# Performance work log

Hardware: AMD Instinct MI355X
Metric: run time of the kernel (lower is better)

## Reference

```python
import jax, jax.numpy as jnp
import numpy as np

DIM, NH, T_MAX = 1024, 16, 2048
HD = DIM // NH
EPS = 1e-6


def _rope_tables(T, hd, dtype=jnp.float32):
    inv_freq = 1.0 / (10000.0 ** (jnp.arange(0, hd, 2, dtype=jnp.float32) / hd))
    t = jnp.arange(T, dtype=jnp.float32)
    freqs = jnp.outer(t, inv_freq)                 # [T, hd/2]
    emb = jnp.concatenate([freqs, freqs], axis=-1)  # [T, hd]
    return jnp.cos(emb).astype(dtype), jnp.sin(emb).astype(dtype)


def _rotate_half(x):
    x1, x2 = jnp.split(x, 2, axis=-1)
    return jnp.concatenate([-x2, x1], axis=-1)


def _rmsnorm(x, g):
    rms = jnp.sqrt(jnp.mean(x * x, axis=-1, keepdims=True) + EPS)
    return x / rms * g


def setup_inputs() -> dict:
    key = jax.random.key(0)
    ks = jax.random.split(key, 10)
    B, T, C = 4, 2048, DIM
    s = 1.0 / np.sqrt(C)
    x = jax.random.normal(ks[0], (B, T, C), dtype=jnp.float32)
    mask = jnp.tril(jnp.ones((T, T), dtype=jnp.int32))[None, None, :, :]
    wq = jax.random.normal(ks[1], (C, C), jnp.float32) * s
    wk = jax.random.normal(ks[2], (C, C), jnp.float32) * s
    wv = jax.random.normal(ks[3], (C, C), jnp.float32) * s
    wo = jax.random.normal(ks[4], (C, C), jnp.float32) * s
    w1 = jax.random.normal(ks[5], (C, 4 * C), jnp.float32) * s
    w2 = jax.random.normal(ks[6], (4 * C, C), jnp.float32) * (1.0 / np.sqrt(4 * C))
    w3 = jax.random.normal(ks[7], (C, 4 * C), jnp.float32) * s
    g1 = jnp.ones((C,), jnp.float32)
    g2 = jnp.ones((C,), jnp.float32)
    return {"x": x, "mask": mask, "g1": g1, "wq": wq, "wk": wk, "wv": wv,
            "wo": wo, "g2": g2, "w1": w1, "w2": w2, "w3": w3}


def reference(x, mask, g1, wq, wk, wv, wo, g2, w1, w2, w3):
    B, T, C = x.shape
    scale = HD ** -0.5
    # --- attention sublayer ---
    h = _rmsnorm(x, g1)
    q = (h @ wq).reshape(B, T, NH, HD)
    k = (h @ wk).reshape(B, T, NH, HD)
    v = (h @ wv).reshape(B, T, NH, HD)
    cos, sin = _rope_tables(T, HD, x.dtype)
    cos = cos[None, :, None, :]
    sin = sin[None, :, None, :]
    q = q * cos + _rotate_half(q) * sin
    k = k * cos + _rotate_half(k) * sin
    attn = jnp.einsum("bthd,bshd->bhts", q, k) * scale  # [B,H,T,T]
    attn = jnp.where(mask == 0, -jnp.inf, attn)
    attn = jax.nn.softmax(attn, axis=-1)
    o = jnp.einsum("bhts,bshd->bthd", attn, v).reshape(B, T, C)
    x = x + o @ wo
    # --- SwiGLU FFN sublayer ---
    h = _rmsnorm(x, g2)
    x = x + (jax.nn.silu(h @ w1) * (h @ w3)) @ w2
    return x
```

## Files before the change

### kernel.cpp

```cpp
#include <hip/hip_runtime.h>
#include <cstdint>

typedef unsigned short u16;
typedef __attribute__((ext_vector_type(8))) short bf16x8;
typedef __attribute__((ext_vector_type(4))) float f32x4;

__device__ __forceinline__ u16 f2b(float f) {
  union { float f; unsigned u; } c; c.f = f;
  unsigned u = c.u;
  return (u16)((u + 0x7FFFu + ((u >> 16) & 1u)) >> 16);
}
__device__ __forceinline__ float b2f(u16 b) {
  union { unsigned u; float f; } c; c.u = ((unsigned)b) << 16;
  return c.f;
}

typedef __attribute__((address_space(1))) void gv_t;
typedef __attribute__((address_space(3))) void lv_t;
__device__ __forceinline__ void gload_lds16(const void* g, void* l) {
  __builtin_amdgcn_global_load_lds((gv_t*)g, (lv_t*)l, 16, 0, 0);
}

__global__ void transpose_f2b(const float* __restrict__ in, u16* __restrict__ out,
                              int R, int C) {
  __shared__ float t[32][33];
  const int c0 = blockIdx.x * 32, r0 = blockIdx.y * 32;
  const int tx = threadIdx.x, ty = threadIdx.y;
#pragma unroll
  for (int i = 0; i < 4; ++i)
    t[ty + 8 * i][tx] = in[(size_t)(r0 + ty + 8 * i) * C + c0 + tx];
  __syncthreads();
#pragma unroll
  for (int i = 0; i < 4; ++i)
    out[(size_t)(c0 + ty + 8 * i) * R + r0 + tx] = f2b(t[tx][ty + 8 * i]);
}

__global__ __launch_bounds__(256) void rmsnorm_k(const float* __restrict__ x,
                                                 const float* __restrict__ g,
                                                 u16* __restrict__ out) {
  const int row = blockIdx.x, tid = threadIdx.x;
  const float4 v = ((const float4*)x)[(size_t)row * 256 + tid];
  float ss = v.x * v.x + v.y * v.y + v.z * v.z + v.w * v.w;
#pragma unroll
  for (int off = 1; off < 64; off <<= 1) ss += __shfl_xor(ss, off, 64);
  __shared__ float red[4];
  if ((tid & 63) == 0) red[tid >> 6] = ss;
  __syncthreads();
  const float mean = (red[0] + red[1] + red[2] + red[3]) * (1.0f / 1024.0f);
  const float rinv = 1.0f / sqrtf(mean + 1e-6f);
  const float4 gv = ((const float4*)g)[tid];
  u16* o = out + (size_t)row * 1024 + tid * 4;
  o[0] = f2b(v.x * rinv * gv.x);
  o[1] = f2b(v.y * rinv * gv.y);
  o[2] = f2b(v.z * rinv * gv.z);
  o[3] = f2b(v.w * rinv * gv.w);
}

__global__ __launch_bounds__(256) void rope_k(u16* __restrict__ qkv) {
  const int i = blockIdx.x * 256 + threadIdx.x;
  const int d = i & 31;
  const int h = (i >> 5) & 15;
  const int bt = i >> 9;
  const int t = bt & 2047;
  const float inv = exp2f((float)d * -0.4152410118609203f);
  const float th = (float)t * inv;
  float s, c;
  sincosf(th, &s, &c);
  size_t base = (size_t)bt * 3072 + h * 64 + d;
#pragma unroll
  for (int half = 0; half < 2; ++half) {
    const float x1 = b2f(qkv[base]);
    const float x2 = b2f(qkv[base + 32]);
    qkv[base]      = f2b(x1 * c - x2 * s);
    qkv[base + 32] = f2b(x2 * c + x1 * s);
    base += 1024;
  }
}

__global__ void vtrans_k(const u16* __restrict__ qkv, u16* __restrict__ VT) {
  __shared__ u16 tl[32][34];
  const int t0 = blockIdx.x * 32;
  const int bh = blockIdx.y >> 1;
  const int d0 = (blockIdx.y & 1) * 32;
  const int b = bh >> 4, h = bh & 15;
  const int tx = threadIdx.x, ty = threadIdx.y;
  const u16* src = qkv + (size_t)(b * 2048 + t0) * 3072 + 2048 + h * 64 + d0;
#pragma unroll
  for (int i = 0; i < 4; ++i)
    tl[ty + 8 * i][tx] = src[(size_t)(ty + 8 * i) * 3072 + tx];
  __syncthreads();
  u16* dst = VT + ((size_t)bh * 64 + d0) * 2048 + t0;
#pragma unroll
  for (int i = 0; i < 4; ++i)
    dst[(size_t)(ty + 8 * i) * 2048 + tx] = tl[tx][ty + 8 * i];
}

template <int EPI>
__global__ __launch_bounds__(256)
void gemm_bt(const u16* __restrict__ A, const u16* __restrict__ BT,
             void* __restrict__ Cout, const float* __restrict__ resid,
             int M, int N, int K, int lda) {
  __shared__ alignas(16) u16 As[128 * 32];
  __shared__ alignas(16) u16 Bs[128 * 32];
  const int tid = threadIdx.x;
  const int wave = tid >> 6, lane = tid & 63;
  const int wr = wave >> 1, wc = wave & 1;
  const int l15 = lane & 15, quad = lane >> 4;
  const int bm = blockIdx.x * 128, bn = blockIdx.y * 128;

  f32x4 acc[4][4];
#pragma unroll
  for (int i = 0; i < 4; ++i)
#pragma unroll
    for (int j = 0; j < 4; ++j) acc[i][j] = (f32x4){0.f, 0.f, 0.f, 0.f};

  const int srow = wave * 32 + (lane >> 2);
  const int scol = (lane & 3) * 8;
  const u16* gA0 = A + (size_t)(bm + srow) * lda + scol;
  const u16* gA1 = gA0 + (size_t)16 * lda;
  const u16* gB0 = BT + (size_t)(bn + srow) * K + scol;
  const u16* gB1 = gB0 + (size_t)16 * K;
  u16* lA0 = As + wave * 1024; u16* lA1 = lA0 + 512;
  u16* lB0 = Bs + wave * 1024; u16* lB1 = lB0 + 512;

  const u16* pa = As + (wr * 64 + l15) * 32 + quad * 8;
  const u16* pb = Bs + (wc * 64 + l15) * 32 + quad * 8;

  for (int kt = 0; kt < K; kt += 32) {
    gload_lds16(gA0 + kt, lA0);
    gload_lds16(gA1 + kt, lA1);
    gload_lds16(gB0 + kt, lB0);
    gload_lds16(gB1 + kt, lB1);
    __syncthreads();
    bf16x8 af[4], bfv[4];
#pragma unroll
    for (int i = 0; i < 4; ++i) af[i] = *(const bf16x8*)(pa + i * 512);
#pragma unroll
    for (int j = 0; j < 4; ++j) bfv[j] = *(const bf16x8*)(pb + j * 512);
#pragma unroll
    for (int i = 0; i < 4; ++i)
#pragma unroll
      for (int j = 0; j < 4; ++j)
        acc[i][j] = __builtin_amdgcn_mfma_f32_16x16x32_bf16(af[i], bfv[j], acc[i][j], 0, 0, 0);
    __syncthreads();
  }

#pragma unroll
  for (int i = 0; i < 4; ++i) {
    const int gr = bm + wr * 64 + i * 16 + quad * 4;
#pragma unroll
    for (int j = 0; j < 4; ++j) {
      const int gc = bn + wc * 64 + j * 16 + l15;
#pragma unroll
      for (int r = 0; r < 4; ++r) {
        const size_t off = (size_t)(gr + r) * N + gc;
        if (EPI == 0) {
          ((u16*)Cout)[off] = f2b(acc[i][j][r]);
        } else {
          ((float*)Cout)[off] = resid[off] + acc[i][j][r];
        }
      }
    }
  }
}

template <int EPI>
__global__ __launch_bounds__(512, 2)
void gemm256(const u16* __restrict__ A, const u16* __restrict__ BT,
             void* __restrict__ Cout, const float* __restrict__ resid,
             int M, int N, int K, int lda) {
  __shared__ alignas(16) u16 LDS[65536];
  char* const ldsc = (char*)LDS;
  const int tid = threadIdx.x;
  const int wave = tid >> 6, lane = tid & 63;
  const int wr = wave >> 2, wc = wave & 3;
  const int l15 = lane & 15, quad = lane >> 4;
  const int bm = blockIdx.x * 256, bn = blockIdx.y * 256;
  const int NT = K >> 6;

  const int swz = (l15 & 8) << 2;
  const int aoff = (((wr * 64 + l15) * 64 + quad * 16) ^ swz);
  const int boff = (((wc * 32 + l15) * 64 + quad * 16) ^ swz) + 65536;

  const int kperm = ((lane & 3) ^ ((lane >> 5) << 1)) * 8;
  const u16* sA = A + (size_t)(bm + wave * 16 + (lane >> 2)) * lda + kperm;
  const u16* sB = BT + (size_t)(bn + wave * 16 + (lane >> 2)) * K + kperm;
  const size_t hA = (size_t)128 * lda;
  const size_t hB = (size_t)128 * K;
  const int dstW = wave * 1024;

  f32x4 acc[8][4];
#pragma unroll
  for (int m = 0; m < 8; ++m)
#pragma unroll
    for (int n = 0; n < 4; ++n) acc[m][n] = (f32x4){0.f, 0.f, 0.f, 0.f};
  bf16x8 a[4][2], b[4][2];

#define STAGE(kt_, slot_, buf_)                                               \
  if ((kt_) < NT) {                                                           \
    const u16* s_ = (((slot_) & 1) ? sB + ((size_t)((slot_) >> 1)) * hB       \
                                   : sA + ((size_t)((slot_) >> 1)) * hA) +    \
                    (size_t)(kt_) * 64;                                       \
    char* d_ = ldsc + (((slot_) & 1) ? 65536 : 0) + (buf_) * 32768 +          \
               ((slot_) >> 1) * 16384 + dstW;                                 \
    gload_lds16(s_, d_);                                                      \
    gload_lds16(s_ + 32, d_ + 8192);                                          \
  }

#define LOAD_A(mh_, buf_)                                                     \
  _Pragma("unroll") for (int mf = 0; mf < 4; ++mf)                            \
      _Pragma("unroll") for (int kk = 0; kk < 2; ++kk)                        \
          a[mf][kk] = *(const bf16x8*)(ldsc + aoff + (buf_) * 32768 +         \
                                       (mh_) * 16384 + kk * 8192 + mf * 1024);

#define LOAD_B2(buf_)                                                         \
  _Pragma("unroll") for (int nh = 0; nh < 2; ++nh)                            \
      _Pragma("unroll") for (int nf = 0; nf < 2; ++nf)                        \
          _Pragma("unroll") for (int kk = 0; kk < 2; ++kk)                    \
              b[nh * 2 + nf][kk] =                                            \
                  *(const bf16x8*)(ldsc + boff + (buf_) * 32768 +             \
                                   nh * 16384 + kk * 8192 + nf * 1024);

#define MMA2(mh_)                                                             \
  __builtin_amdgcn_s_setprio(1);                                              \
  _Pragma("unroll") for (int mf = 0; mf < 4; ++mf)                            \
      _Pragma("unroll") for (int n = 0; n < 4; ++n)                           \
          _Pragma("unroll") for (int kk = 0; kk < 2; ++kk)                    \
              acc[(mh_) * 4 + mf][n] =                                        \
                  __builtin_amdgcn_mfma_f32_16x16x32_bf16(                    \
                      a[mf][kk], b[n][kk], acc[(mh_) * 4 + mf][n], 0, 0, 0);  \
  __builtin_amdgcn_s_setprio(0);

#define BAR() __builtin_amdgcn_s_barrier()
#define DRAIN_LGKM()                                                          \
  {                                                                           \
    asm volatile("s_waitcnt lgkmcnt(0)" ::: "memory");                        \
    __builtin_amdgcn_sched_barrier(0);                                        \
  }

  STAGE(0, 0, 0); STAGE(0, 1, 0); STAGE(0, 3, 0);
  STAGE(0, 2, 0);
  STAGE(1, 0, 1); STAGE(1, 1, 1); STAGE(1, 3, 1);
  asm volatile("s_waitcnt vmcnt(8)" ::: "memory");
  BAR();

  for (int t = 0; t < NT; ++t) {
    const int bsel = t & 1;
    LOAD_A(0, bsel); LOAD_B2(bsel);
    STAGE(t + 1, 2, bsel ^ 1);
    BAR(); DRAIN_LGKM(); MMA2(0);
    if (t == NT - 1) { asm volatile("s_waitcnt vmcnt(0)" ::: "memory"); }
    else             { asm volatile("s_waitcnt vmcnt(8)" ::: "memory"); }
    BAR();
    LOAD_A(1, bsel);
    STAGE(t + 2, 0, bsel); STAGE(t + 2, 1, bsel); STAGE(t + 2, 3, bsel);
    BAR(); DRAIN_LGKM(); MMA2(1);
    if (t < NT - 2) {
      asm volatile("s_waitcnt vmcnt(8)" ::: "memory");
      BAR();
    } else if (t == NT - 2) {
      asm volatile("s_waitcnt vmcnt(2)" ::: "memory");
      BAR();
    }
  }
#undef STAGE
#undef LOAD_A
#undef LOAD_B2
#undef MMA2

#pragma unroll
  for (int m = 0; m < 8; ++m) {
    const int gr = bm + (m >> 2) * 128 + wr * 64 + (m & 3) * 16 + quad * 4;
#pragma unroll
    for (int n = 0; n < 4; ++n) {
      const int gc = bn + (n >> 1) * 128 + wc * 32 + (n & 1) * 16 + l15;
#pragma unroll
      for (int r = 0; r < 4; ++r) {
        const size_t off = (size_t)(gr + r) * N + gc;
        if (EPI == 0) {
          ((u16*)Cout)[off] = f2b(acc[m][n][r]);
        } else {
          ((float*)Cout)[off] = resid[off] + acc[m][n][r];
        }
      }
    }
  }
#undef BAR
#undef DRAIN_LGKM
}

template <int EPI>
__global__ __launch_bounds__(512, 2)
void gemm256n(const u16* __restrict__ A, const u16* __restrict__ BT,
              void* __restrict__ Cout, const float* __restrict__ resid,
              int M, int N, int K, int lda) {
  __shared__ alignas(16) u16 LDS[49152];
  char* const ldsc = (char*)LDS;
  const int tid = threadIdx.x;
  const int wave = tid >> 6, lane = tid & 63;
  const int wr = wave >> 2, wc = wave & 3;
  const int l15 = lane & 15, quad = lane >> 4;
  const int bm = blockIdx.x * 256, bn = blockIdx.y * 128;
  const int NT = K >> 6;

  const int swz = (l15 & 8) << 2;
  const int aoff = (((wr * 64 + l15) * 64 + quad * 16) ^ swz);
  const int boff = (((wc * 32 + l15) * 64 + quad * 16) ^ swz) + 65536;

  const int kperm = ((lane & 3) ^ ((lane >> 5) << 1)) * 8;
  const u16* sA = A + (size_t)(bm + wave * 16 + (lane >> 2)) * lda + kperm;
  const u16* sB = BT + (size_t)(bn + wave * 16 + (lane >> 2)) * K + kperm;
  const size_t hA = (size_t)128 * lda;
  const int dstW = wave * 1024;

  f32x4 acc[8][2];
#pragma unroll
  for (int m = 0; m < 8; ++m)
#pragma unroll
    for (int n = 0; n < 2; ++n) acc[m][n] = (f32x4){0.f, 0.f, 0.f, 0.f};
  bf16x8 a[4][2], b[2][2];

#define STAGE_A(kt_, half_, buf_)                                             \
  if ((kt_) < NT) {                                                           \
    const u16* s_ = sA + (size_t)(half_) * hA + (size_t)(kt_) * 64;           \
    char* d_ = ldsc + (buf_) * 32768 + (half_) * 16384 + dstW;                \
    gload_lds16(s_, d_);                                                      \
    gload_lds16(s_ + 32, d_ + 8192);                                          \
  }
#define STAGE_B(kt_, buf_)                                                    \
  if ((kt_) < NT) {                                                           \
    const u16* s_ = sB + (size_t)(kt_) * 64;                                  \
    char* d_ = ldsc + 65536 + (buf_) * 16384 + dstW;                          \
    gload_lds16(s_, d_);                                                      \
    gload_lds16(s_ + 32, d_ + 8192);                                          \
  }
#define LOAD_A(mh_, buf_)                                                     \
  _Pragma("unroll") for (int mf = 0; mf < 4; ++mf)                            \
      _Pragma("unroll") for (int kk = 0; kk < 2; ++kk)                        \
          a[mf][kk] = *(const bf16x8*)(ldsc + aoff + (buf_) * 32768 +         \
                                       (mh_) * 16384 + kk * 8192 + mf * 1024);
#define LOAD_B(buf_)                                                          \
  _Pragma("unroll") for (int nf = 0; nf < 2; ++nf)                            \
      _Pragma("unroll") for (int kk = 0; kk < 2; ++kk)                        \
          b[nf][kk] = *(const bf16x8*)(ldsc + boff + (buf_) * 16384 +         \
                                       kk * 8192 + nf * 1024);
#define MMA(mh_)                                                              \
  __builtin_amdgcn_s_setprio(1);                                              \
  _Pragma("unroll") for (int mf = 0; mf < 4; ++mf)                            \
      _Pragma("unroll") for (int nf = 0; nf < 2; ++nf)                        \
          _Pragma("unroll") for (int kk = 0; kk < 2; ++kk)                    \
              acc[(mh_) * 4 + mf][nf] =                                       \
                  __builtin_amdgcn_mfma_f32_16x16x32_bf16(                    \
                      a[mf][kk], b[nf][kk], acc[(mh_) * 4 + mf][nf], 0, 0, 0);\
  __builtin_amdgcn_s_setprio(0);
#define BAR() __builtin_amdgcn_s_barrier()
#define DRAIN_LGKM()                                                          \
  {                                                                           \
    asm volatile("s_waitcnt lgkmcnt(0)" ::: "memory");                        \
    __builtin_amdgcn_sched_barrier(0);                                        \
  }

  STAGE_A(0, 0, 0); STAGE_B(0, 0);
  STAGE_A(0, 1, 0);
  STAGE_A(1, 0, 1); STAGE_B(1, 1);
  asm volatile("s_waitcnt vmcnt(6)" ::: "memory");
  BAR();

  for (int t = 0; t < NT; ++t) {
    const int bsel = t & 1;
    LOAD_A(0, bsel); LOAD_B(bsel);
    STAGE_A(t + 1, 1, bsel ^ 1);
    BAR(); DRAIN_LGKM(); MMA(0);
    if (t == NT - 1) { asm volatile("s_waitcnt vmcnt(0)" ::: "memory"); }
    else             { asm volatile("s_waitcnt vmcnt(6)" ::: "memory"); }
    BAR();
    LOAD_A(1, bsel);
    STAGE_A(t + 2, 0, bsel); STAGE_B(t + 2, bsel);
    BAR(); DRAIN_LGKM(); MMA(1);
    if (t == NT - 2)     { asm volatile("s_waitcnt vmcnt(2)" ::: "memory"); }
    else if (t < NT - 2) { asm volatile("s_waitcnt vmcnt(6)" ::: "memory"); }
    BAR();
  }
#undef STAGE_A
#undef STAGE_B
#undef LOAD_A
#undef LOAD_B
#undef MMA
#undef BAR
#undef DRAIN_LGKM

#pragma unroll
  for (int m = 0; m < 8; ++m) {
    const int gr = bm + (m >> 2) * 128 + wr * 64 + (m & 3) * 16 + quad * 4;
#pragma unroll
    for (int n = 0; n < 2; ++n) {
      const int gc = bn + wc * 32 + n * 16 + l15;
#pragma unroll
      for (int r = 0; r < 4; ++r) {
        const size_t off = (size_t)(gr + r) * N + gc;
        if (EPI == 0) {
          ((u16*)Cout)[off] = f2b(acc[m][n][r]);
        } else {
          ((float*)Cout)[off] = resid[off] + acc[m][n][r];
        }
      }
    }
  }
}

__global__ __launch_bounds__(256)
void attn_kernel(const u16* __restrict__ QKV, const u16* __restrict__ VT,
                 u16* __restrict__ O, float* __restrict__ Opart,
                 float* __restrict__ Spart) {
  const int T = 2048, stQ = 3072;
  const int tid = threadIdx.x, wave = tid >> 6, lane = tid & 63;
  const int l15 = lane & 15, quad = lane >> 4;

  const int xi = (int)blockIdx.x;
  const bool split = (xi < 22);
  const int qt = split ? (15 - (xi >> 1)) : (26 - xi);
  const int chunk = split ? (xi & 1) : 0;
  const int len = split ? (qt + 1) : (2 * qt + 2);
  const int kt0 = chunk * (qt + 1);
  const int ktEnd = kt0 + len;

  const int qb0 = qt * 128;
  const int bh = blockIdx.y, b = bh >> 4, h = bh & 15;
  const float sc2 = 0.125f * 1.44269504088896f;
  const float M0 = 32.0f;

  __shared__ alignas(16) u16 Kf[2][8 * 512];
  __shared__ alignas(16) u16 Vf[2][8 * 512];
  __shared__ alignas(16) u16 Pl[4][2][16 * 72];

  const u16* Qb  = QKV + (size_t)b * T * stQ + h * 64;
  const u16* Kb  = Qb + 1024;
  const u16* VTb = VT + (size_t)bh * 64 * T;

  const int r0 = qb0 + wave * 16;
  const int r1 = r0 + 64;
  const u16* qp0 = Qb + (size_t)(r0 + l15) * stQ + quad * 8;
  const u16* qp1 = Qb + (size_t)(r1 + l15) * stQ + quad * 8;
  const bf16x8 qf00 = *(const bf16x8*)qp0;
  const bf16x8 qf01 = *(const bf16x8*)(qp0 + 32);
  const bf16x8 qf10 = *(const bf16x8*)qp1;
  const bf16x8 qf11 = *(const bf16x8*)(qp1 + 32);

  bf16x8 ones;
#pragma unroll
  for (int j = 0; j < 8; ++j) ones[j] = (short)0x3F80;

  const u16* kS = Kb + (size_t)(wave * 16 + l15) * stQ + quad * 8;
  const u16* vS = VTb + (size_t)(wave * 16 + l15) * T + quad * 8;

  f32x4 o0[4], o1[4], sum0, sum1;
#pragma unroll
  for (int c = 0; c < 4; ++c) {
    o0[c] = (f32x4){0.f, 0.f, 0.f, 0.f};
    o1[c] = (f32x4){0.f, 0.f, 0.f, 0.f};
  }
  sum0 = (f32x4){0.f, 0.f, 0.f, 0.f};
  sum1 = (f32x4){0.f, 0.f, 0.f, 0.f};

  u16* pw0 = &Pl[wave][0][0];
  u16* pw1 = &Pl[wave][1][0];

  gload_lds16(kS + (size_t)(kt0 * 64) * stQ,      &Kf[0][(wave * 2 + 0) * 512]);
  gload_lds16(kS + (size_t)(kt0 * 64) * stQ + 32, &Kf[0][(wave * 2 + 1) * 512]);
  gload_lds16(vS + (size_t)(kt0 * 64),            &Vf[0][(wave * 2 + 0) * 512]);
  gload_lds16(vS + (size_t)(kt0 * 64) + 32,       &Vf[0][(wave * 2 + 1) * 512]);

  for (int kt = kt0; kt < ktEnd; ++kt) {
    const int kb0 = kt * 64;
    const int buf = (kt - kt0) & 1;
    __builtin_amdgcn_sched_barrier(0);
    if (kt + 1 < ktEnd) {
      const size_t kb1 = (size_t)(kb0 + 64);
      gload_lds16(kS + kb1 * stQ,      &Kf[buf ^ 1][(wave * 2 + 0) * 512]);
      gload_lds16(kS + kb1 * stQ + 32, &Kf[buf ^ 1][(wave * 2 + 1) * 512]);
      gload_lds16(vS + kb1,            &Vf[buf ^ 1][(wave * 2 + 0) * 512]);
      gload_lds16(vS + kb1 + 32,       &Vf[buf ^ 1][(wave * 2 + 1) * 512]);
      asm volatile("s_waitcnt vmcnt(4)" ::: "memory");
    } else {
      asm volatile("s_waitcnt vmcnt(0)" ::: "memory");
    }
    __builtin_amdgcn_s_barrier();
    __builtin_amdgcn_sched_barrier(0);

    bf16x8 kf[8], vf[8];
#pragma unroll
    for (int g = 0; g < 8; ++g) {
      kf[g] = *(const bf16x8*)(&Kf[buf][g * 512 + lane * 8]);
      vf[g] = *(const bf16x8*)(&Vf[buf][g * 512 + lane * 8]);
    }

    const bool act0 = (kb0 <= r0 + 15);

    {
      f32x4 s[4];
      __builtin_amdgcn_s_setprio(1);
#pragma unroll
      for (int jj = 0; jj < 4; ++jj) {
        s[jj] = (f32x4){0.f, 0.f, 0.f, 0.f};
        s[jj] = __builtin_amdgcn_mfma_f32_16x16x32_bf16(qf10, kf[jj * 2 + 0], s[jj], 0, 0, 0);
        s[jj] = __builtin_amdgcn_mfma_f32_16x16x32_bf16(qf11, kf[jj * 2 + 1], s[jj], 0, 0, 0);
      }
      __builtin_amdgcn_s_setprio(0);
      if (kb0 + 63 > r1) {
#pragma unroll
        for (int jj = 0; jj < 4; ++jj)
#pragma unroll
          for (int r = 0; r < 4; ++r) {
            const bool msk = (kb0 + jj * 16 + l15) > (r1 + quad * 4 + r);
            const float a = msk ? -1e30f : (s[jj][r] * sc2 - M0);
            pw1[(quad * 4 + r) * 72 + jj * 16 + l15] = f2b(exp2f(a));
          }
      } else {
#pragma unroll
        for (int jj = 0; jj < 4; ++jj)
#pragma unroll
          for (int r = 0; r < 4; ++r)
            pw1[(quad * 4 + r) * 72 + jj * 16 + l15] =
                f2b(exp2f(s[jj][r] * sc2 - M0));
      }
    }
    if (act0) {
      f32x4 s[4];
      __builtin_amdgcn_s_setprio(1);
#pragma unroll
      for (int jj = 0; jj < 4; ++jj) {
        s[jj] = (f32x4){0.f, 0.f, 0.f, 0.f};
        s[jj] = __builtin_amdgcn_mfma_f32_16x16x32_bf16(qf00, kf[jj * 2 + 0], s[jj], 0, 0, 0);
        s[jj] = __builtin_amdgcn_mfma_f32_16x16x32_bf16(qf01, kf[jj * 2 + 1], s[jj], 0, 0, 0);
      }
      __builtin_amdgcn_s_setprio(0);
      if (kb0 + 63 > r0) {
#pragma unroll
        for (int jj = 0; jj < 4; ++jj)
#pragma unroll
          for (int r = 0; r < 4; ++r) {
            const bool msk = (kb0 + jj * 16 + l15) > (r0 + quad * 4 + r);
            const float a = msk ? -1e30f : (s[jj][r] * sc2 - M0);
            pw0[(quad * 4 + r) * 72 + jj * 16 + l15] = f2b(exp2f(a));
          }
      } else {
#pragma unroll
        for (int jj = 0; jj < 4; ++jj)
#pragma unroll
          for (int r = 0; r < 4; ++r)
            pw0[(quad * 4 + r) * 72 + jj * 16 + l15] =
                f2b(exp2f(s[jj][r] * sc2 - M0));
      }
    }

    const bf16x8 pf10 = *(const bf16x8*)(pw1 + l15 * 72 + quad * 8);
    const bf16x8 pf11 = *(const bf16x8*)(pw1 + l15 * 72 + 32 + quad * 8);
    __builtin_amdgcn_s_setprio(1);
#pragma unroll
    for (int c = 0; c < 4; ++c) {
      o1[c] = __builtin_amdgcn_mfma_f32_16x16x32_bf16(pf10, vf[c * 2 + 0], o1[c], 0, 0, 0);
      o1[c] = __builtin_amdgcn_mfma_f32_16x16x32_bf16(pf11, vf[c * 2 + 1], o1[c], 0, 0, 0);
    }
    sum1 = __builtin_amdgcn_mfma_f32_16x16x32_bf16(pf10, ones, sum1, 0, 0, 0);
    sum1 = __builtin_amdgcn_mfma_f32_16x16x32_bf16(pf11, ones, sum1, 0, 0, 0);
    __builtin_amdgcn_s_setprio(0);
    if (act0) {
      const bf16x8 pf00 = *(const bf16x8*)(pw0 + l15 * 72 + quad * 8);
      const bf16x8 pf01 = *(const bf16x8*)(pw0 + l15 * 72 + 32 + quad * 8);
      __builtin_amdgcn_s_setprio(1);
#pragma unroll
      for (int c = 0; c < 4; ++c) {
        o0[c] = __builtin_amdgcn_mfma_f32_16x16x32_bf16(pf00, vf[c * 2 + 0], o0[c], 0, 0, 0);
        o0[c] = __builtin_amdgcn_mfma_f32_16x16x32_bf16(pf01, vf[c * 2 + 1], o0[c], 0, 0, 0);
      }
      sum0 = __builtin_amdgcn_mfma_f32_16x16x32_bf16(pf00, ones, sum0, 0, 0, 0);
      sum0 = __builtin_amdgcn_mfma_f32_16x16x32_bf16(pf01, ones, sum0, 0, 0, 0);
      __builtin_amdgcn_s_setprio(0);
    }
    __builtin_amdgcn_s_barrier();
  }

  if (split) {
    const int pi = (bh * 11 + (qt - 5)) * 2 + chunk;
    float* Po = Opart + (size_t)pi * 8192;
    float* Ps = Spart + (size_t)pi * 128;
    const int lr0 = wave * 16 + quad * 4;
#pragma unroll
    for (int c = 0; c < 4; ++c)
#pragma unroll
      for (int r = 0; r < 4; ++r) {
        Po[(lr0 + r) * 64 + c * 16 + l15]      = o0[c][r];
        Po[(64 + lr0 + r) * 64 + c * 16 + l15] = o1[c][r];
      }
    if (l15 == 0) {
#pragma unroll
      for (int r = 0; r < 4; ++r) {
        Ps[lr0 + r]      = sum0[r];
        Ps[64 + lr0 + r] = sum1[r];
      }
    }
  } else {
    float i0[4], i1[4];
#pragma unroll
    for (int r = 0; r < 4; ++r) { i0[r] = 1.f / sum0[r]; i1[r] = 1.f / sum1[r]; }
    u16* op0 = O + ((size_t)(b * T) + r0 + quad * 4) * 1024 + h * 64 + l15;
    u16* op1 = O + ((size_t)(b * T) + r1 + quad * 4) * 1024 + h * 64 + l15;
#pragma unroll
    for (int c = 0; c < 4; ++c)
#pragma unroll
      for (int r = 0; r < 4; ++r) {
        op0[(size_t)r * 1024 + c * 16] = f2b(o0[c][r] * i0[r]);
        op1[(size_t)r * 1024 + c * 16] = f2b(o1[c][r] * i1[r]);
      }
  }
}

__global__ __launch_bounds__(256)
void attn_combine(const float* __restrict__ Opart, const float* __restrict__ Spart,
                  u16* __restrict__ O) {
  const int sp = blockIdx.x;
  const int bh = sp / 11, qt = 5 + (sp % 11);
  const int b = bh >> 4, h = bh & 15;
  const int t = threadIdx.x;
  const int row = t >> 1, ch = (t & 1) * 32;
  const size_t p0 = (size_t)(2 * sp) * 8192, p1 = p0 + 8192;
  const float s = Spart[(size_t)(2 * sp) * 128 + row] +
                  Spart[(size_t)(2 * sp) * 128 + 128 + row];
  const float inv = 1.f / s;
  const float4* A  = (const float4*)(Opart + p0 + row * 64 + ch);
  const float4* Bv = (const float4*)(Opart + p1 + row * 64 + ch);
  u16* op = O + ((size_t)(b * 2048) + qt * 128 + row) * 1024 + h * 64 + ch;
#pragma unroll
  for (int j = 0; j < 8; ++j) {
    const float4 a = A[j], bb = Bv[j];
    op[j * 4 + 0] = f2b((a.x + bb.x) * inv);
    op[j * 4 + 1] = f2b((a.y + bb.y) * inv);
    op[j * 4 + 2] = f2b((a.z + bb.z) * inv);
    op[j * 4 + 3] = f2b((a.w + bb.w) * inv);
  }
}

__global__ __launch_bounds__(256) void gate_k(u16* __restrict__ a13) {
  const size_t i = (size_t)blockIdx.x * 256 + threadIdx.x;
  const size_t row = i >> 9, c8 = (i & 511) * 8;
  u16* p1v = a13 + row * 8192 + c8;
  const u16* p3v = p1v + 4096;
  uint4 u1 = *(uint4*)p1v;
  const uint4 u3 = *(const uint4*)p3v;
  u16* p1 = (u16*)&u1;
  const u16* p3 = (const u16*)&u3;
#pragma unroll
  for (int j = 0; j < 8; ++j) {
    const float a = b2f(p1[j]);
    const float g = b2f(p3[j]);
    const float s = a / (1.f + __expf(-a));
    p1[j] = f2b(s * g);
  }
  *(uint4*)p1v = u1;
}

extern "C" void kernel_launch(void* const* d_in, const int* in_sizes, int n_in,
                              void* d_out, int out_size, void* d_ws, size_t ws_size,
                              hipStream_t stream) {
  const float* x  = (const float*)d_in[0];
  const float* g1 = (const float*)d_in[2];
  const float* wq = (const float*)d_in[3];
  const float* wk = (const float*)d_in[4];
  const float* wv = (const float*)d_in[5];
  const float* wo = (const float*)d_in[6];
  const float* g2 = (const float*)d_in[7];
  const float* w1 = (const float*)d_in[8];
  const float* w2 = (const float*)d_in[9];
  const float* w3 = (const float*)d_in[10];
  float* out = (float*)d_out;

  const int T = 2048, NH = 16, B = 4;
  const int M = B * T;
  const size_t MB = 1ull << 20;

  char* ws = (char*)d_ws;
  u16* hb    = (u16*)(ws);
  u16* wqkvT = (u16*)(ws + 16 * MB);
  u16* woT   = (u16*)(ws + 22 * MB);
  u16* w13T  = (u16*)(ws + 24 * MB);
  u16* w2T   = (u16*)(ws + 40 * MB);
  u16* qkv   = (u16*)(ws + 48 * MB);
  u16* VT    = (u16*)(ws + 96 * MB);
  u16* Ob    = (u16*)(ws + 112 * MB);
  u16* a13   = (u16*)(ws + 48 * MB);
  float* Opart = (float*)(ws + 128 * MB);
  float* Spart = Opart + (size_t)1408 * 8192;

  const dim3 tb(32, 8);
  transpose_f2b<<<dim3(32, 32),  tb, 0, stream>>>(wq, wqkvT,              1024, 1024);
  transpose_f2b<<<dim3(32, 32),  tb, 0, stream>>>(wk, wqkvT + 1024*1024,  1024, 1024);
  transpose_f2b<<<dim3(32, 32),  tb, 0, stream>>>(wv, wqkvT + 2048*1024,  1024, 1024);
  transpose_f2b<<<dim3(32, 32),  tb, 0, stream>>>(wo, woT, 1024, 1024);
  transpose_f2b<<<dim3(128, 32), tb, 0, stream>>>(w1, w13T,               1024, 4096);
  transpose_f2b<<<dim3(128, 32), tb, 0, stream>>>(w3, w13T + 4096*1024,   1024, 4096);
  transpose_f2b<<<dim3(32, 128), tb, 0, stream>>>(w2, w2T, 4096, 1024);

  rmsnorm_k<<<M, 256, 0, stream>>>(x, g1, hb);

  gemm256<0><<<dim3(32, 12), 512, 0, stream>>>(hb, wqkvT, qkv, nullptr, M, 3072, 1024, 1024);

  rope_k<<<16384, 256, 0, stream>>>(qkv);
  vtrans_k<<<dim3(64, 128), tb, 0, stream>>>(qkv, VT);

  attn_kernel<<<dim3(27, B * NH), 256, 0, stream>>>(qkv, VT, Ob, Opart, Spart);
  attn_combine<<<dim3(704), 256, 0, stream>>>(Opart, Spart, Ob);

  gemm256n<1><<<dim3(32, 8), 512, 0, stream>>>(Ob, woT, out, x, M, 1024, 1024, 1024);

  rmsnorm_k<<<M, 256, 0, stream>>>(out, g2, hb);

  gemm256<0><<<dim3(32, 32), 512, 0, stream>>>(hb, w13T, a13, nullptr, M, 8192, 1024, 1024);

  gate_k<<<16384, 256, 0, stream>>>(a13);

  gemm256n<1><<<dim3(32, 8), 512, 0, stream>>>(a13, w2T, out, out, M, 1024, 4096, 8192);
}
```

Baseline: 674.7 us.

## Fuse SwiGLU gate into the W1/W3 GEMM epilogue

```diff
diff --git a/kernel.cpp b/kernel.cpp
--- a/kernel.cpp
+++ b/kernel.cpp
@@ -93,75 +93,6 @@
 #pragma unroll
   for (int i = 0; i < 4; ++i)
     dst[(size_t)(ty + 8 * i) * 2048 + tx] = tl[tx][ty + 8 * i];
-}
-
-template <int EPI>
-__global__ __launch_bounds__(256)
-void gemm_bt(const u16* __restrict__ A, const u16* __restrict__ BT,
-             void* __restrict__ Cout, const float* __restrict__ resid,
-             int M, int N, int K, int lda) {
-  __shared__ alignas(16) u16 As[128 * 32];
-  __shared__ alignas(16) u16 Bs[128 * 32];
-  const int tid = threadIdx.x;
-  const int wave = tid >> 6, lane = tid & 63;
-  const int wr = wave >> 1, wc = wave & 1;
-  const int l15 = lane & 15, quad = lane >> 4;
-  const int bm = blockIdx.x * 128, bn = blockIdx.y * 128;
-
-  f32x4 acc[4][4];
-#pragma unroll
-  for (int i = 0; i < 4; ++i)
-#pragma unroll
-    for (int j = 0; j < 4; ++j) acc[i][j] = (f32x4){0.f, 0.f, 0.f, 0.f};
-
-  const int srow = wave * 32 + (lane >> 2);
-  const int scol = (lane & 3) * 8;
-  const u16* gA0 = A + (size_t)(bm + srow) * lda + scol;
-  const u16* gA1 = gA0 + (size_t)16 * lda;
-  const u16* gB0 = BT + (size_t)(bn + srow) * K + scol;
-  const u16* gB1 = gB0 + (size_t)16 * K;
-  u16* lA0 = As + wave * 1024; u16* lA1 = lA0 + 512;
-  u16* lB0 = Bs + wave * 1024; u16* lB1 = lB0 + 512;
-
-  const u16* pa = As + (wr * 64 + l15) * 32 + quad * 8;
-  const u16* pb = Bs + (wc * 64 + l15) * 32 + quad * 8;
-
-  for (int kt = 0; kt < K; kt += 32) {
-    gload_lds16(gA0 + kt, lA0);
-    gload_lds16(gA1 + kt, lA1);
-    gload_lds16(gB0 + kt, lB0);
-    gload_lds16(gB1 + kt, lB1);
-    __syncthreads();
-    bf16x8 af[4], bfv[4];
-#pragma unroll
-    for (int i = 0; i < 4; ++i) af[i] = *(const bf16x8*)(pa + i * 512);
-#pragma unroll
-    for (int j = 0; j < 4; ++j) bfv[j] = *(const bf16x8*)(pb + j * 512);
-#pragma unroll
-    for (int i = 0; i < 4; ++i)
-#pragma unroll
-      for (int j = 0; j < 4; ++j)
-        acc[i][j] = __builtin_amdgcn_mfma_f32_16x16x32_bf16(af[i], bfv[j], acc[i][j], 0, 0, 0);
-    __syncthreads();
-  }
-
-#pragma unroll
-  for (int i = 0; i < 4; ++i) {
-    const int gr = bm + wr * 64 + i * 16 + quad * 4;
-#pragma unroll
-    for (int j = 0; j < 4; ++j) {
-      const int gc = bn + wc * 64 + j * 16 + l15;
-#pragma unroll
-      for (int r = 0; r < 4; ++r) {
-        const size_t off = (size_t)(gr + r) * N + gc;
-        if (EPI == 0) {
-          ((u16*)Cout)[off] = f2b(acc[i][j][r]);
-        } else {
-          ((float*)Cout)[off] = resid[off] + acc[i][j][r];
-        }
-      }
-    }
-  }
 }
 
 template <int EPI>
@@ -287,6 +218,146 @@
   }
 #undef BAR
 #undef DRAIN_LGKM
+}
+
+__global__ __launch_bounds__(512, 2)
+void gemm256g(const u16* __restrict__ A, const u16* __restrict__ B1T,
+              const u16* __restrict__ B3T, u16* __restrict__ Cout,
+              int Ncols, int K, int lda) {
+  __shared__ alignas(16) u16 LDS[65536];
+  char* const ldsc = (char*)LDS;
+  const int tid = threadIdx.x;
+  const int wave = tid >> 6, lane = tid & 63;
+  const int wr = wave >> 2, wc = wave & 3;
+  const int l15 = lane & 15, quad = lane >> 4;
+  const int bm = blockIdx.x * 256, bn = blockIdx.y * 128;
+  const int NT = K >> 6;
+
+  const int swz = (l15 & 8) << 2;
+  const int aoff  = (((wr * 64 + l15) * 64 + quad * 16) ^ swz);
+  const int b1off = (((wc * 32 + l15) * 64 + quad * 16) ^ swz) + 65536;
+
+  const int kperm = ((lane & 3) ^ ((lane >> 5) << 1)) * 8;
+  const u16* sA  = A   + (size_t)(bm + wave * 16 + (lane >> 2)) * lda + kperm;
+  const u16* sB1 = B1T + (size_t)(bn + wave * 16 + (lane >> 2)) * K + kperm;
+  const u16* sB3 = B3T + (size_t)(bn + wave * 16 + (lane >> 2)) * K + kperm;
+  const size_t hA = (size_t)128 * lda;
+  const int dstW = wave * 1024;
+
+  f32x4 acc1[8][2], acc3[8][2];
+#pragma unroll
+  for (int m = 0; m < 8; ++m)
+#pragma unroll
+    for (int n = 0; n < 2; ++n) {
+      acc1[m][n] = (f32x4){0.f, 0.f, 0.f, 0.f};
+      acc3[m][n] = (f32x4){0.f, 0.f, 0.f, 0.f};
+    }
+  bf16x8 a[4][2], b1[2][2], b3[2][2];
+
+#define STAGE_A(kt_, half_, buf_)                                             \
+  if ((kt_) < NT) {                                                           \
+    const u16* s_ = sA + (size_t)(half_) * hA + (size_t)(kt_) * 64;           \
+    char* d_ = ldsc + (buf_) * 32768 + (half_) * 16384 + dstW;                \
+    gload_lds16(s_, d_);                                                      \
+    gload_lds16(s_ + 32, d_ + 8192);                                          \
+  }
+#define STAGE_B1(kt_, buf_)                                                   \
+  if ((kt_) < NT) {                                                           \
+    const u16* s_ = sB1 + (size_t)(kt_) * 64;                                 \
+    char* d_ = ldsc + 65536 + (buf_) * 16384 + dstW;                          \
+    gload_lds16(s_, d_);                                                      \
+    gload_lds16(s_ + 32, d_ + 8192);                                          \
+  }
+#define STAGE_B3(kt_, buf_)                                                   \
+  if ((kt_) < NT) {                                                           \
+    const u16* s_ = sB3 + (size_t)(kt_) * 64;                                 \
+    char* d_ = ldsc + 98304 + (buf_) * 16384 + dstW;                          \
+    gload_lds16(s_, d_);                                                      \
+    gload_lds16(s_ + 32, d_ + 8192);                                          \
+  }
+#define LOAD_A(mh_, buf_)                                                     \
+  _Pragma("unroll") for (int mf = 0; mf < 4; ++mf)                            \
+      _Pragma("unroll") for (int kk = 0; kk < 2; ++kk)                        \
+          a[mf][kk] = *(const bf16x8*)(ldsc + aoff + (buf_) * 32768 +         \
+                                       (mh_) * 16384 + kk * 8192 + mf * 1024);
+#define LOAD_B13(buf_)                                                        \
+  _Pragma("unroll") for (int nf = 0; nf < 2; ++nf)                            \
+      _Pragma("unroll") for (int kk = 0; kk < 2; ++kk) {                      \
+        b1[nf][kk] = *(const bf16x8*)(ldsc + b1off + (buf_) * 16384 +         \
+                                      kk * 8192 + nf * 1024);                 \
+        b3[nf][kk] = *(const bf16x8*)(ldsc + b1off + 32768 +                  \
+                                      (buf_) * 16384 + kk * 8192 +            \
+                                      nf * 1024);                             \
+      }
+#define MMAG(mh_)                                                             \
+  __builtin_amdgcn_s_setprio(1);                                              \
+  _Pragma("unroll") for (int mf = 0; mf < 4; ++mf)                            \
+      _Pragma("unroll") for (int nf = 0; nf < 2; ++nf)                        \
+          _Pragma("unroll") for (int kk = 0; kk < 2; ++kk) {                  \
+            acc1[(mh_) * 4 + mf][nf] =                                        \
+                __builtin_amdgcn_mfma_f32_16x16x32_bf16(                      \
+                    a[mf][kk], b1[nf][kk], acc1[(mh_) * 4 + mf][nf], 0, 0, 0);\
+            acc3[(mh_) * 4 + mf][nf] =                                        \
+                __builtin_amdgcn_mfma_f32_16x16x32_bf16(                      \
+                    a[mf][kk], b3[nf][kk], acc3[(mh_) * 4 + mf][nf], 0, 0, 0);\
+          }                                                                   \
+  __builtin_amdgcn_s_setprio(0);
+#define BAR() __builtin_amdgcn_s_barrier()
+#define DRAIN_LGKM()                                                          \
+  {                                                                           \
+    asm volatile("s_waitcnt lgkmcnt(0)" ::: "memory");                        \
+    __builtin_amdgcn_sched_barrier(0);                                        \
+  }
+
+  STAGE_A(0, 0, 0); STAGE_B1(0, 0); STAGE_B3(0, 0);
+  STAGE_A(0, 1, 0);
+  STAGE_A(1, 0, 1); STAGE_B1(1, 1); STAGE_B3(1, 1);
+  asm volatile("s_waitcnt vmcnt(8)" ::: "memory");
+  BAR();
+
+  for (int t = 0; t < NT; ++t) {
+    const int bsel = t & 1;
+    LOAD_A(0, bsel); LOAD_B13(bsel);
+    STAGE_A(t + 1, 1, bsel ^ 1);
+    BAR(); DRAIN_LGKM(); MMAG(0);
+    if (t == NT - 1) { asm volatile("s_waitcnt vmcnt(0)" ::: "memory"); }
+    else             { asm volatile("s_waitcnt vmcnt(8)" ::: "memory"); }
+    BAR();
+    LOAD_A(1, bsel);
+    STAGE_A(t + 2, 0, bsel); STAGE_B1(t + 2, bsel); STAGE_B3(t + 2, bsel);
+    BAR(); DRAIN_LGKM(); MMAG(1);
+    if (t < NT - 2) {
+      asm volatile("s_waitcnt vmcnt(8)" ::: "memory");
+      BAR();
+    } else if (t == NT - 2) {
+      asm volatile("s_waitcnt vmcnt(2)" ::: "memory");
+      BAR();
+    }
+  }
+#undef STAGE_A
+#undef STAGE_B1
+#undef STAGE_B3
+#undef LOAD_A
+#undef LOAD_B13
+#undef MMAG
+#undef BAR
+#undef DRAIN_LGKM
+
+#pragma unroll
+  for (int m = 0; m < 8; ++m) {
+    const int gr = bm + (m >> 2) * 128 + wr * 64 + (m & 3) * 16 + quad * 4;
+#pragma unroll
+    for (int n = 0; n < 2; ++n) {
+      const int gc = bn + wc * 32 + n * 16 + l15;
+#pragma unroll
+      for (int r = 0; r < 4; ++r) {
+        const float v1 = acc1[m][n][r];
+        const float v3 = acc3[m][n][r];
+        const float s = v1 / (1.f + __expf(-v1));
+        Cout[(size_t)(gr + r) * Ncols + gc] = f2b(s * v3);
+      }
+    }
+  }
 }
 
 template <int EPI>
@@ -640,25 +711,6 @@
   }
 }
 
-__global__ __launch_bounds__(256) void gate_k(u16* __restrict__ a13) {
-  const size_t i = (size_t)blockIdx.x * 256 + threadIdx.x;
-  const size_t row = i >> 9, c8 = (i & 511) * 8;
-  u16* p1v = a13 + row * 8192 + c8;
-  const u16* p3v = p1v + 4096;
-  uint4 u1 = *(uint4*)p1v;
-  const uint4 u3 = *(const uint4*)p3v;
-  u16* p1 = (u16*)&u1;
-  const u16* p3 = (const u16*)&u3;
-#pragma unroll
-  for (int j = 0; j < 8; ++j) {
-    const float a = b2f(p1[j]);
-    const float g = b2f(p3[j]);
-    const float s = a / (1.f + __expf(-a));
-    p1[j] = f2b(s * g);
-  }
-  *(uint4*)p1v = u1;
-}
-
 extern "C" void kernel_launch(void* const* d_in, const int* in_sizes, int n_in,
                               void* d_out, int out_size, void* d_ws, size_t ws_size,
                               hipStream_t stream) {
@@ -687,7 +739,7 @@
   u16* qkv   = (u16*)(ws + 48 * MB);
   u16* VT    = (u16*)(ws + 96 * MB);
   u16* Ob    = (u16*)(ws + 112 * MB);
-  u16* a13   = (u16*)(ws + 48 * MB);
+  u16* a13g  = (u16*)(ws + 48 * MB);
   float* Opart = (float*)(ws + 128 * MB);
   float* Spart = Opart + (size_t)1408 * 8192;
 
@@ -714,9 +766,8 @@
 
   rmsnorm_k<<<M, 256, 0, stream>>>(out, g2, hb);
 
-  gemm256<0><<<dim3(32, 32), 512, 0, stream>>>(hb, w13T, a13, nullptr, M, 8192, 1024, 1024);
-
-  gate_k<<<16384, 256, 0, stream>>>(a13);
-
-  gemm256n<1><<<dim3(32, 8), 512, 0, stream>>>(a13, w2T, out, out, M, 1024, 4096, 8192);
-}
+  gemm256g<<<dim3(32, 32), 512, 0, stream>>>(hb, w13T, w13T + (size_t)4096 * 1024,
+                                             a13g, 4096, 1024, 1024);
+
+  gemm256n<1><<<dim3(32, 8), 512, 0, stream>>>(a13g, w2T, out, out, M, 1024, 4096, 4096);
+}
```

After: 637.7 us (median of 2 runs). 5.5% less time.
